# Kernel tuning notes

Measured on AMD Instinct MI355X. Metric: run time of the kernel, lower is better.

The kernel has to match this reference:

```python
import jax, jax.numpy as jnp
import numpy as np

TAU = 0.2
N_CLUSTERS = 8
FOURIER_K = 8
LATENT_DIM = 64
B = 131072
N_MINUTES = 1440
TWO_PI = 2.0 * np.pi


def setup_inputs() -> dict:
    key = jax.random.key(0)
    ks = jax.random.split(key, 6)
    item_static_emb = jax.random.normal(ks[0], (B, LATENT_DIM), dtype=jnp.float32) * 0.1
    thetas = jax.random.uniform(ks[1], (B,), dtype=jnp.float32) * TWO_PI  # absolute time phase in [0, 2pi)
    cluster_prototypes = jax.random.normal(ks[2], (N_CLUSTERS, LATENT_DIM), dtype=jnp.float32) * 0.1
    fourier_a0 = jax.random.normal(ks[3], (N_CLUSTERS, LATENT_DIM), dtype=jnp.float32) * 0.1
    fourier_a = jax.random.normal(ks[4], (N_CLUSTERS, FOURIER_K, LATENT_DIM), dtype=jnp.float32) * 0.1
    fourier_b = jax.random.normal(ks[5], (N_CLUSTERS, FOURIER_K, LATENT_DIM), dtype=jnp.float32) * 0.1
    return {
        "item_static_emb": item_static_emb,
        "thetas": thetas,
        "cluster_prototypes": cluster_prototypes,
        "fourier_a0": fourier_a0,
        "fourier_a": fourier_a,
        "fourier_b": fourier_b,
    }


def reference(item_static_emb, thetas, cluster_prototypes, fourier_a0, fourier_a, fourier_b):
    # Soft cluster routing: (B, n_clusters)
    scores = jnp.matmul(item_static_emb, cluster_prototypes.T) / TAU
    P = jax.nn.softmax(scores, axis=1)

    # Time-indexed minute bucket; torch builds tables from linspace(0, 2pi, 1440)
    # so the angle for bucket m is m * 2pi/1439.
    minute_indices = jnp.clip((thetas / TWO_PI * N_MINUTES).astype(jnp.int32), 0, N_MINUTES - 1)
    k_seq = jnp.arange(1, FOURIER_K + 1, dtype=jnp.float32)  # (K,)
    angles = minute_indices.astype(jnp.float32) * (TWO_PI / (N_MINUTES - 1))  # (B,)
    k_angles = angles[:, None] * k_seq[None, :]  # (B, K)
    cos_vals = jnp.cos(k_angles)  # (B, K)
    sin_vals = jnp.sin(k_angles)  # (B, K)

    # Fourier-series evaluation per cluster: (B, n_clusters, d)
    a_term = jnp.einsum('bk,nkd->bnd', cos_vals, fourier_a)
    b_term = jnp.einsum('bk,nkd->bnd', sin_vals, fourier_b)
    F_theta = fourier_a0[None, :, :] + a_term + b_term  # (B, n_clusters, d)

    # Softmax-weighted mixture combine: (B, d)
    item_dynamic_emb = jnp.einsum('bn,bnd->bd', P, F_theta)
    return item_dynamic_emb, P
```

## Files before the change

### kernel.cpp

```cpp
#include <hip/hip_runtime.h>
#include <math.h>

#define D 64
#define NC 8
#define FK 8
#define NMIN 1440
#define TWO_PI_F 6.28318530717958647692f

__global__ __launch_bounds__(256) void build_table_kernel(
    const float* __restrict__ a0,
    const float* __restrict__ fa,
    const float* __restrict__ fb,
    float* __restrict__ T)
{
    const int m = blockIdx.x;
    const int t = threadIdx.x;
    const int d  = t & (D - 1);
    const int n0 = t >> 6;
    const float angle = (float)m * (TWO_PI_F / (float)(NMIN - 1));

    float c[FK], s[FK];
    float s1, c1;
    sincosf(angle, &s1, &c1);
    c[0] = c1; s[0] = s1;
    {
        const float tw = 2.0f * c1;
        float cp = 1.0f, sp = 0.0f;
        float cc = c1, ss = s1;
#pragma unroll
        for (int k = 1; k < FK; ++k) {
            const float cn = fmaf(tw, cc, -cp);
            const float sn = fmaf(tw, ss, -sp);
            cp = cc; sp = ss; cc = cn; ss = sn;
            c[k] = cc; s[k] = ss;
        }
    }

#pragma unroll
    for (int j = 0; j < 2; ++j) {
        const int n = n0 + 4 * j;
        float v = a0[n * D + d];
#pragma unroll
        for (int k = 0; k < FK; ++k) {
            v = fmaf(c[k], fa[(n * FK + k) * D + d], v);
            v = fmaf(s[k], fb[(n * FK + k) * D + d], v);
        }
        T[(m * NC + n) * D + d] = v;
    }
}

__device__ __forceinline__ float grp16_allreduce_sum(float v) {
    int t;
    t = __builtin_amdgcn_update_dpp(0, __float_as_int(v), 0xB1, 0xF, 0xF, true);
    v += __int_as_float(t);
    t = __builtin_amdgcn_update_dpp(0, __float_as_int(v), 0x4E, 0xF, 0xF, true);
    v += __int_as_float(t);
    t = __builtin_amdgcn_update_dpp(0, __float_as_int(v), 0x141, 0xF, 0xF, true);
    v += __int_as_float(t);
    t = __builtin_amdgcn_update_dpp(0, __float_as_int(v), 0x128, 0xF, 0xF, true);
    v += __int_as_float(t);
    return v;
}

__global__ __launch_bounds__(256) void mix_kernel16(
    const float* __restrict__ emb,
    const float* __restrict__ thetas,
    const float* __restrict__ proto,
    const float* __restrict__ T,
    float* __restrict__ out_emb,
    float* __restrict__ out_P,
    int B)
{
    __shared__ float4 sproto[NC * (D / 4)];
    if (threadIdx.x < NC * (D / 4)) {
        sproto[threadIdx.x] = ((const float4*)proto)[threadIdx.x];
    }
    __syncthreads();

    const int t = blockIdx.x * 256 + threadIdx.x;
    const int b = t >> 4;
    const int i = t & 15;
    if (b >= B) return;

    const float4 ev = ((const float4*)emb)[(size_t)b * (D / 4) + i];

    float sc[NC];
#pragma unroll
    for (int n = 0; n < NC; ++n) {
        const float4 pv = sproto[n * (D / 4) + i];
        float v = ev.x * pv.x;
        v = fmaf(ev.y, pv.y, v);
        v = fmaf(ev.z, pv.z, v);
        v = fmaf(ev.w, pv.w, v);
        sc[n] = v;
    }

#pragma unroll
    for (int n = 0; n < NC; ++n) {
        sc[n] = grp16_allreduce_sum(sc[n]);
    }

    float mx = -1e30f;
#pragma unroll
    for (int n = 0; n < NC; ++n) { sc[n] *= 5.0f; mx = fmaxf(mx, sc[n]); }
    float sum = 0.0f;
#pragma unroll
    for (int n = 0; n < NC; ++n) { sc[n] = __expf(sc[n] - mx); sum += sc[n]; }
    const float inv = 1.0f / sum;
#pragma unroll
    for (int n = 0; n < NC; ++n) sc[n] *= inv;

    const float th = thetas[b];
    int m = (int)((th / TWO_PI_F) * (float)NMIN);
    m = m < 0 ? 0 : (m > NMIN - 1 ? NMIN - 1 : m);

    const float4* __restrict__ t4 = (const float4*)(T + (size_t)m * NC * D);
    float4 acc = make_float4(0.f, 0.f, 0.f, 0.f);
#pragma unroll
    for (int n = 0; n < NC; ++n) {
        const float4 tv = t4[n * (D / 4) + i];
        const float pw = sc[n];
        acc.x = fmaf(pw, tv.x, acc.x);
        acc.y = fmaf(pw, tv.y, acc.y);
        acc.z = fmaf(pw, tv.z, acc.z);
        acc.w = fmaf(pw, tv.w, acc.w);
    }

    ((float4*)out_emb)[(size_t)b * (D / 4) + i] = acc;

    if (i == 0) {
        ((float4*)out_P)[(size_t)b * 2 + 0] = make_float4(sc[0], sc[1], sc[2], sc[3]);
    } else if (i == 8) {
        ((float4*)out_P)[(size_t)b * 2 + 1] = make_float4(sc[4], sc[5], sc[6], sc[7]);
    }
}

__global__ __launch_bounds__(256) void fused_fallback(
    const float* __restrict__ emb,
    const float* __restrict__ thetas,
    const float* __restrict__ proto,
    const float* __restrict__ a0,
    const float* __restrict__ fa,
    const float* __restrict__ fb,
    float* __restrict__ out_emb,
    float* __restrict__ out_P,
    int B)
{
    __shared__ float sp[NC * D];
    __shared__ float sa0[NC * D];
    __shared__ float sfa[NC * FK * D];
    __shared__ float sfb[NC * FK * D];
    for (int i = threadIdx.x; i < NC * D; i += 256) { sp[i] = proto[i]; sa0[i] = a0[i]; }
    for (int i = threadIdx.x; i < NC * FK * D; i += 256) { sfa[i] = fa[i]; sfb[i] = fb[i]; }
    __syncthreads();

    const int b = blockIdx.x * 256 + threadIdx.x;
    if (b >= B) return;

    const float4* __restrict__ e4  = (const float4*)(emb + (size_t)b * D);
    const float4* sp4  = (const float4*)sp;
    const float4* sa04 = (const float4*)sa0;
    const float4* sfa4 = (const float4*)sfa;
    const float4* sfb4 = (const float4*)sfb;

    float sc[NC];
#pragma unroll
    for (int n = 0; n < NC; ++n) sc[n] = 0.0f;
#pragma unroll
    for (int i = 0; i < D / 4; ++i) {
        const float4 ev = e4[i];
#pragma unroll
        for (int n = 0; n < NC; ++n) {
            const float4 pv = sp4[n * (D / 4) + i];
            sc[n] = fmaf(ev.x, pv.x, sc[n]);
            sc[n] = fmaf(ev.y, pv.y, sc[n]);
            sc[n] = fmaf(ev.z, pv.z, sc[n]);
            sc[n] = fmaf(ev.w, pv.w, sc[n]);
        }
    }
    float mx = -1e30f;
#pragma unroll
    for (int n = 0; n < NC; ++n) { sc[n] *= 5.0f; mx = fmaxf(mx, sc[n]); }
    float sum = 0.0f;
#pragma unroll
    for (int n = 0; n < NC; ++n) { sc[n] = __expf(sc[n] - mx); sum += sc[n]; }
    const float inv = 1.0f / sum;
#pragma unroll
    for (int n = 0; n < NC; ++n) sc[n] *= inv;

    const float th = thetas[b];
    int m = (int)((th / TWO_PI_F) * (float)NMIN);
    m = m < 0 ? 0 : (m > NMIN - 1 ? NMIN - 1 : m);
    const float angle = (float)m * (TWO_PI_F / (float)(NMIN - 1));
    float c[FK], s[FK];
#pragma unroll
    for (int k = 0; k < FK; ++k) sincosf(angle * (float)(k + 1), &s[k], &c[k]);

    float4 acc[D / 4];
#pragma unroll
    for (int i = 0; i < D / 4; ++i) acc[i] = make_float4(0.f, 0.f, 0.f, 0.f);
#pragma unroll
    for (int n = 0; n < NC; ++n) {
        const float pw = sc[n];
#pragma unroll
        for (int i = 0; i < D / 4; ++i) {
            float4 v = sa04[n * (D / 4) + i];
#pragma unroll
            for (int k = 0; k < FK; ++k) {
                const float4 av = sfa4[(n * FK + k) * (D / 4) + i];
                const float4 bv = sfb4[(n * FK + k) * (D / 4) + i];
                v.x = fmaf(c[k], av.x, v.x); v.x = fmaf(s[k], bv.x, v.x);
                v.y = fmaf(c[k], av.y, v.y); v.y = fmaf(s[k], bv.y, v.y);
                v.z = fmaf(c[k], av.z, v.z); v.z = fmaf(s[k], bv.z, v.z);
                v.w = fmaf(c[k], av.w, v.w); v.w = fmaf(s[k], bv.w, v.w);
            }
            acc[i].x = fmaf(pw, v.x, acc[i].x);
            acc[i].y = fmaf(pw, v.y, acc[i].y);
            acc[i].z = fmaf(pw, v.z, acc[i].z);
            acc[i].w = fmaf(pw, v.w, acc[i].w);
        }
    }
    float4* o4 = (float4*)(out_emb + (size_t)b * D);
#pragma unroll
    for (int i = 0; i < D / 4; ++i) o4[i] = acc[i];
    float4* op = (float4*)(out_P + (size_t)b * NC);
    op[0] = make_float4(sc[0], sc[1], sc[2], sc[3]);
    op[1] = make_float4(sc[4], sc[5], sc[6], sc[7]);
}

extern "C" void kernel_launch(void* const* d_in, const int* in_sizes, int n_in,
                              void* d_out, int out_size, void* d_ws, size_t ws_size,
                              hipStream_t stream)
{
    const float* emb    = (const float*)d_in[0];
    const float* thetas = (const float*)d_in[1];
    const float* proto  = (const float*)d_in[2];
    const float* a0     = (const float*)d_in[3];
    const float* fa     = (const float*)d_in[4];
    const float* fb     = (const float*)d_in[5];

    const int B = in_sizes[0] / D;
    float* out_emb = (float*)d_out;
    float* out_P   = (float*)d_out + (size_t)B * D;

    const size_t table_bytes = (size_t)NMIN * NC * D * sizeof(float);

    if (ws_size >= table_bytes) {
        float* T = (float*)d_ws;
        build_table_kernel<<<NMIN, 256, 0, stream>>>(a0, fa, fb, T);
        const long long total_threads = (long long)B * 16;
        const int blocks = (int)((total_threads + 255) / 256);
        mix_kernel16<<<blocks, 256, 0, stream>>>(emb, thetas, proto, T, out_emb, out_P, B);
    } else {
        const int blocks = (B + 255) / 256;
        fused_fallback<<<blocks, 256, 0, stream>>>(emb, thetas, proto, a0, fa, fb,
                                                   out_emb, out_P, B);
    }
}
```

Baseline: 31.37 us.

## Store Fourier lookup table in fp16 and prefetch table rows early

```diff
diff --git a/kernel.cpp b/kernel.cpp
--- a/kernel.cpp
+++ b/kernel.cpp
@@ -1,4 +1,5 @@
 #include <hip/hip_runtime.h>
+#include <hip/hip_fp16.h>
 #include <math.h>
 
 #define D 64
@@ -7,11 +8,13 @@
 #define NMIN 1440
 #define TWO_PI_F 6.28318530717958647692f
 
+#define TSZ ((size_t)NMIN * NC * D)
+
 __global__ __launch_bounds__(256) void build_table_kernel(
     const float* __restrict__ a0,
     const float* __restrict__ fa,
     const float* __restrict__ fb,
-    float* __restrict__ T)
+    __half* __restrict__ T)
 {
     const int m = blockIdx.x;
     const int t = threadIdx.x;
@@ -45,7 +48,7 @@
             v = fmaf(c[k], fa[(n * FK + k) * D + d], v);
             v = fmaf(s[k], fb[(n * FK + k) * D + d], v);
         }
-        T[(m * NC + n) * D + d] = v;
+        T[(size_t)(m * NC + n) * D + d] = __float2half(v);
     }
 }
 
@@ -66,7 +69,7 @@
     const float* __restrict__ emb,
     const float* __restrict__ thetas,
     const float* __restrict__ proto,
-    const float* __restrict__ T,
+    const __half* __restrict__ T,
     float* __restrict__ out_emb,
     float* __restrict__ out_P,
     int B)
@@ -82,7 +85,18 @@
     const int i = t & 15;
     if (b >= B) return;
 
+    const float th = thetas[b];
+    int m = (int)((th / TWO_PI_F) * (float)NMIN);
+    m = m < 0 ? 0 : (m > NMIN - 1 ? NMIN - 1 : m);
+
     const float4 ev = ((const float4*)emb)[(size_t)b * (D / 4) + i];
+
+    const uint2* __restrict__ t2 = (const uint2*)(T + (size_t)m * NC * D);
+    uint2 u[NC];
+#pragma unroll
+    for (int n = 0; n < NC; ++n) {
+        u[n] = t2[n * 16 + i];
+    }
 
     float sc[NC];
 #pragma unroll
@@ -110,20 +124,16 @@
 #pragma unroll
     for (int n = 0; n < NC; ++n) sc[n] *= inv;
 
-    const float th = thetas[b];
-    int m = (int)((th / TWO_PI_F) * (float)NMIN);
-    m = m < 0 ? 0 : (m > NMIN - 1 ? NMIN - 1 : m);
-
-    const float4* __restrict__ t4 = (const float4*)(T + (size_t)m * NC * D);
     float4 acc = make_float4(0.f, 0.f, 0.f, 0.f);
 #pragma unroll
     for (int n = 0; n < NC; ++n) {
-        const float4 tv = t4[n * (D / 4) + i];
         const float pw = sc[n];
-        acc.x = fmaf(pw, tv.x, acc.x);
-        acc.y = fmaf(pw, tv.y, acc.y);
-        acc.z = fmaf(pw, tv.z, acc.z);
-        acc.w = fmaf(pw, tv.w, acc.w);
+        const float2 a01 = __half22float2(*(const __half2*)&u[n].x);
+        const float2 a23 = __half22float2(*(const __half2*)&u[n].y);
+        acc.x = fmaf(pw, a01.x, acc.x);
+        acc.y = fmaf(pw, a01.y, acc.y);
+        acc.z = fmaf(pw, a23.x, acc.z);
+        acc.w = fmaf(pw, a23.y, acc.w);
     }
 
     ((float4*)out_emb)[(size_t)b * (D / 4) + i] = acc;
@@ -243,10 +253,10 @@
     float* out_emb = (float*)d_out;
     float* out_P   = (float*)d_out + (size_t)B * D;
 
-    const size_t table_bytes = (size_t)NMIN * NC * D * sizeof(float);
+    const size_t table_bytes = TSZ * sizeof(__half);
 
     if (ws_size >= table_bytes) {
-        float* T = (float*)d_ws;
+        __half* T = (__half*)d_ws;
         build_table_kernel<<<NMIN, 256, 0, stream>>>(a0, fa, fb, T);
         const long long total_threads = (long long)B * 16;
         const int blocks = (int)((total_threads + 255) / 256);
```

Result: faster. 26.58 us (median of 2 runs) (-15.3%).
